# Kernel tuning notes

Hardware: AMD Instinct MI355X
Metric: run time of the kernel (lower is better)

The kernel has to match this reference:

```python
import jax, jax.numpy as jnp
import numpy as np
import math

NEG = -10000.0  # module uses -10000, not -inf


def setup_inputs() -> dict:
    key = jax.random.key(0)
    k1, k2, k3 = jax.random.split(key, 3)
    B, Sq, Sk, H, Hkv, D = 2, 2048, 2048, 16, 4, 64
    q = jax.random.normal(k1, (B, Sq, H, D), dtype=jnp.float32)
    kv = jax.random.normal(k2, (B, Sk, 2, Hkv, D), dtype=jnp.float32)
    key_padding_mask = jax.random.randint(k3, (B, Sk), 0, 2) > 0  # True = valid key
    return {"q": q, "kv": kv, "key_padding_mask": key_padding_mask}


def reference(q, kv, key_padding_mask):
    B, Sq, H, D = q.shape
    Sk, Hkv = kv.shape[1], kv.shape[3]
    if Hkv != H:
        # einops repeat '... hkv d -> ... (hkv g) d': each kv head repeated g times contiguously
        kv = jnp.repeat(kv, H // Hkv, axis=3)
    k, v = kv[:, :, 0], kv[:, :, 1]  # [B, Sk, H, D] each
    scale = 1.0 / math.sqrt(D)
    scores = jnp.einsum('bthd,bshd->bhts', q, k * scale)  # [B, H, Sq, Sk]
    # key padding: additive 0 where valid, -10000 where padded
    pad = jnp.where(key_padding_mask, 0.0, NEG).astype(scores.dtype)
    scores = scores + pad[:, None, None, :]
    # causal mask: cols > rows + Sk - Sq gets replaced (not added) with -10000
    rows = jnp.arange(Sq)[:, None]
    cols = jnp.arange(Sk)[None, :]
    causal_mask = cols > rows + (Sk - Sq)
    scores = jnp.where(causal_mask, NEG, scores)
    attention = jax.nn.softmax(scores, axis=-1).astype(v.dtype)
    # dropout p=0.0 -> identity
    output = jnp.einsum('bhts,bshd->bthd', attention, v)  # [B, Sq, H, D]
    return output
```

## Files before the change

kernel.cpp:

```cpp
#include <hip/hip_runtime.h>
#include <math.h>


typedef __bf16 bf16x4 __attribute__((ext_vector_type(4)));
typedef __bf16 bf16x8 __attribute__((ext_vector_type(8)));
typedef float floatx4 __attribute__((ext_vector_type(4)));
typedef float floatx16 __attribute__((ext_vector_type(16)));

#define B_ 2
#define SQ 2048
#define SK 2048
#define H_ 16
#define HKV 4
#define D_ 64
#define QT 128
#define KT 64
#define PAD 72
#define KVROW 512
#define NEGV (-10000.0f)
#define QSCL 0.18033688f
#define EBIAS 17.3123405f

__global__ __launch_bounds__(256, 2)
void attn_kernel(const float* __restrict__ q,
                 const float* __restrict__ kv,
                 const int* __restrict__ mask,
                 float* __restrict__ out)
{
    __shared__ alignas(16) __bf16 Kt[KT][PAD];
    __shared__ alignas(16) __bf16 Vt[D_][PAD];
    __shared__ alignas(16) __bf16 Pl[4][32][PAD];
    __shared__ float linv[4][32];
    __shared__ float fpart[4][64];
    __shared__ float fw[4][64];
    __shared__ int s_first;

    const int tid  = threadIdx.x;
    const int wave = tid >> 6;
    const int lane = tid & 63;

    if (blockIdx.x >= 512) {
        const int bh = (int)blockIdx.x - 512;
        const int b = bh >> 4, h = bh & 15, hkv = h >> 2;
        if (tid == 0) s_first = SK;
        __syncthreads();
        int local = SK;
        for (int s = tid; s < SK; s += 256)
            if (mask[b * SK + s]) local = min(local, s);
        atomicMin(&s_first, local);
        __syncthreads();
        const int nfirst = s_first;
        if (nfirst == 0) return;

        const float* kvb = kv + (size_t)b * SK * KVROW + hkv * D_;
        const float* vvb = kvb + HKV * D_;
        {
            float a0=0,a1=0,a2=0,a3=0,a4=0,a5=0,a6=0,a7=0;
            const int s0 = wave * 512;
            for (int s = s0; s < s0 + 512; s += 8) {
                a0 += vvb[(size_t)(s+0)*KVROW + lane];
                a1 += vvb[(size_t)(s+1)*KVROW + lane];
                a2 += vvb[(size_t)(s+2)*KVROW + lane];
                a3 += vvb[(size_t)(s+3)*KVROW + lane];
                a4 += vvb[(size_t)(s+4)*KVROW + lane];
                a5 += vvb[(size_t)(s+5)*KVROW + lane];
                a6 += vvb[(size_t)(s+6)*KVROW + lane];
                a7 += vvb[(size_t)(s+7)*KVROW + lane];
            }
            fpart[wave][lane] = ((a0+a1)+(a2+a3)) + ((a4+a5)+(a6+a7));
        }
        __syncthreads();
        const float vtotal = fpart[0][lane]+fpart[1][lane]+fpart[2][lane]+fpart[3][lane];

        for (int R = wave; R < nfirst; R += 4) {
            const float* qrow = q + (((size_t)b * SQ + R) * H_ + h) * D_;
            float mymax = -3.4e38f;
            for (int s = lane; s <= R; s += 64) {
                const float* kp = kvb + (size_t)s * KVROW;
                float dt = 0.f;
                for (int d = 0; d < D_; ++d) dt += qrow[d] * kp[d];
                mymax = fmaxf(mymax, dt * 0.125f + NEGV);
            }
#pragma unroll
            for (int off = 32; off >= 1; off >>= 1)
                mymax = fmaxf(mymax, __shfl_xor(mymax, off, 64));
            const float M = (R < SK - 1) ? fmaxf(mymax, NEGV) : mymax;
            float lsum = 0.f, oacc = 0.f, pref = 0.f;
            for (int s0 = 0; s0 <= R; s0 += 64) {
                int s = s0 + lane;
                float w = 0.f;
                if (s <= R) {
                    const float* kp = kvb + (size_t)s * KVROW;
                    float dt = 0.f;
                    for (int d = 0; d < D_; ++d) dt += qrow[d] * kp[d];
                    w = __expf(dt * 0.125f + NEGV - M);
                    lsum += w;
                }
                fw[wave][lane] = w;
                const int nk = (R - s0 + 1 < 64) ? (R - s0 + 1) : 64;
                for (int j = 0; j < nk; ++j) {
                    const float vj = vvb[(size_t)(s0 + j) * KVROW + lane];
                    oacc += fw[wave][j] * vj;
                    pref += vj;
                }
            }
#pragma unroll
            for (int off = 32; off >= 1; off >>= 1)
                lsum += __shfl_xor(lsum, off, 64);
            const float wn   = __expf(NEGV - M);
            const float ltot = lsum + wn * (float)(SK - 1 - R);
            out[(((size_t)b * SQ + R) * H_ + h) * D_ + lane] =
                (oacc + wn * (vtotal - pref)) / ltot;
        }
        return;
    }

    const int half = lane >> 5;
    const int nn   = lane & 31;

    const int id = (int)blockIdx.x;
    const int bh = id & 31;
    const int y  = id >> 5;
    const int qt = (y < 8) ? 15 - y : y - 8;
    const int b = bh >> 4, h = bh & 15, hkv = h >> 2;
    const int q0 = qt * QT;
    const int qrow_g = q0 + wave * 32 + nn;

    bf16x8 bq[4];
    {
        const float* qp = q + (((size_t)b * SQ + qrow_g) * H_ + h) * D_;
#pragma unroll
        for (int ks = 0; ks < 4; ++ks)
#pragma unroll
            for (int j = 0; j < 8; ++j)
                bq[ks][j] = (__bf16)(qp[ks * 16 + half * 8 + j] * QSCL);
    }

    floatx16 o0, o1;
#pragma unroll
    for (int i = 0; i < 16; ++i) { o0[i] = 0.f; o1[i] = 0.f; }
    float lsum = 0.f;

    const int kkey = tid >> 4;
    const int kd   = (tid & 15) * 4;
    const int vkey = (tid & 15) * 4;
    const int vd   = (tid >> 4) * 4;

    const float* kvb = kv + (size_t)b * SK * KVROW + hkv * D_;

    float4 kreg[4], vreg[4];
    int mreg = 0;

    auto prefetch = [&](int kt) {
        const float* kb = kvb + (size_t)kt * KT * KVROW;
#pragma unroll
        for (int i = 0; i < 4; ++i)
            kreg[i] = *(const float4*)(kb + (kkey + 16 * i) * KVROW + kd);
        const float* vb = kb + HKV * D_;
#pragma unroll
        for (int i = 0; i < 4; ++i)
            vreg[i] = *(const float4*)(vb + (vkey + i) * KVROW + vd);
        mreg = mask[b * SK + kt * KT + lane];
    };

    auto stage = [&]() {
#pragma unroll
        for (int i = 0; i < 4; ++i) {
            bf16x4 t = { (__bf16)kreg[i].x, (__bf16)kreg[i].y,
                         (__bf16)kreg[i].z, (__bf16)kreg[i].w };
            *(bf16x4*)&Kt[kkey + 16 * i][kd] = t;
        }
        const float* vf = (const float*)vreg;
#pragma unroll
        for (int j = 0; j < 4; ++j) {
            bf16x4 t = { (__bf16)vf[0*4+j], (__bf16)vf[1*4+j],
                         (__bf16)vf[2*4+j], (__bf16)vf[3*4+j] };
            *(bf16x4*)&Vt[vd + j][vkey] = t;
        }
    };

    const int nkt = 2 * (qt + 1);
    prefetch(0);

    for (int kt = 0; kt < nkt; ++kt) {
        stage();
        const unsigned long long kept = __ballot(mreg != 0);
        __syncthreads();
        if (kt + 1 < nkt) prefetch(kt + 1);

        const int k0 = kt * KT;
        const bool skipw = (kt == 2*qt + 1) && (wave < 2);
        const bool dg    = (kt == 2*qt) ? (wave < 2) : (kt == 2*qt + 1);

        if (!skipw) {
#pragma unroll
            for (int t2 = 0; t2 < 2; ++t2) {
                floatx16 cst;
#pragma unroll
                for (int i = 0; i < 16; ++i) cst[i] = 0.f;
#pragma unroll
                for (int ks = 0; ks < 4; ++ks) {
                    bf16x8 ak = *(const bf16x8*)&Kt[t2*32 + nn][ks*16 + half*8];
                    cst = __builtin_amdgcn_mfma_f32_32x32x16_bf16(ak, bq[ks], cst, 0, 0, 0);
                }
#pragma unroll
                for (int rq = 0; rq < 4; ++rq) {
                    const int mb = t2*32 + rq*8 + half*4;
                    const unsigned bits = (unsigned)(kept >> mb);
                    bf16x4 pk;
#pragma unroll
                    for (int r = 0; r < 4; ++r) {
                        float p = __builtin_amdgcn_exp2f(cst[rq*4 + r] - EBIAS);
                        if (!((bits >> r) & 1u)) p = 0.f;
                        if (dg && (k0 + mb + r > qrow_g)) p = 0.f;
                        lsum += p;
                        pk[r] = (__bf16)p;
                    }
                    *(bf16x4*)&Pl[wave][nn][mb] = pk;
                }
            }
            bf16x8 ap[4];
#pragma unroll
            for (int ks = 0; ks < 4; ++ks)
                ap[ks] = *(const bf16x8*)&Pl[wave][nn][ks*16 + half*8];
#pragma unroll
            for (int ks = 0; ks < 4; ++ks) {
                bf16x8 bv0 = *(const bf16x8*)&Vt[nn][ks*16 + half*8];
                o0 = __builtin_amdgcn_mfma_f32_32x32x16_bf16(ap[ks], bv0, o0, 0, 0, 0);
                bf16x8 bv1 = *(const bf16x8*)&Vt[32 + nn][ks*16 + half*8];
                o1 = __builtin_amdgcn_mfma_f32_32x32x16_bf16(ap[ks], bv1, o1, 0, 0, 0);
            }
        }
        __syncthreads();
    }

    lsum += __shfl_xor(lsum, 32, 64);
    linv[wave][nn] = (lsum > 0.f) ? 1.f / lsum : 0.f;
#pragma unroll
    for (int rq = 0; rq < 4; ++rq) {
        const int m0 = rq * 8 + half * 4;
        floatx4 li = *(const floatx4*)&linv[wave][m0];
#pragma unroll
        for (int r = 0; r < 4; ++r) {
            if (li[r] != 0.f) {
                const int row = q0 + wave * 32 + m0 + r;
                float* op = out + (((size_t)b * SQ + row) * H_ + h) * D_ + nn;
                op[0]  = o0[rq*4 + r] * li[r];
                op[32] = o1[rq*4 + r] * li[r];
            }
        }
    }
}

extern "C" void kernel_launch(void* const* d_in, const int* in_sizes, int n_in,
                              void* d_out, int out_size, void* d_ws, size_t ws_size,
                              hipStream_t stream) {
    const float* q   = (const float*)d_in[0];
    const float* kv  = (const float*)d_in[1];
    const int* mask  = (const int*)d_in[2];
    float* out       = (float*)d_out;
    attn_kernel<<<dim3(512 + B_ * H_), 256, 0, stream>>>(q, kv, mask, out);
}
```

Measured before the change: 128.9 us.

## Halve query tile and split key tile across wave pairs with LDS reduction

The query tile shrinks from 128 to 64 rows, doubling the block count to 1024 plus 32 fallback blocks. The four waves now form a 2x2 grid: two query halves times two key halves of each 64-key tile. Partial outputs and row sums are combined through a shared-memory reduction unioned with the K/V staging buffers. Launch bounds move to 4 blocks per CU and the special blocks run first. The aim is better occupancy and load balance, at the cost of each K/V tile being loaded twice as often per query row and an extra end-of-kernel reduction.

New measurement: 136.7 us. 1.06x slower.

```diff
diff --git a/kernel.cpp b/kernel.cpp
--- a/kernel.cpp
+++ b/kernel.cpp
@@ -13,34 +13,39 @@
 #define H_ 16
 #define HKV 4
 #define D_ 64
-#define QT 128
+#define QT 64
 #define KT 64
-#define PAD 72
+#define PADK 72
+#define PADP 40
 #define KVROW 512
 #define NEGV (-10000.0f)
 #define QSCL 0.18033688f
 #define EBIAS 17.3123405f
 
-__global__ __launch_bounds__(256, 2)
+__global__ __launch_bounds__(256, 4)
 void attn_kernel(const float* __restrict__ q,
                  const float* __restrict__ kv,
                  const int* __restrict__ mask,
                  float* __restrict__ out)
 {
-    __shared__ alignas(16) __bf16 Kt[KT][PAD];
-    __shared__ alignas(16) __bf16 Vt[D_][PAD];
-    __shared__ alignas(16) __bf16 Pl[4][32][PAD];
-    __shared__ float linv[4][32];
-    __shared__ float fpart[4][64];
-    __shared__ float fw[4][64];
+    __shared__ union {
+        struct { __bf16 Kt[KT][PADK]; __bf16 Vt[D_][PADK]; } m;
+        float Ored[2][32][64];
+        struct { float part[4][64]; float w[4][64]; } f;
+    } u;
+    __shared__ alignas(16) __bf16 Pl[4][32][PADP];
+    __shared__ float lpart[2][2][32];
+    __shared__ float linv[2][32];
     __shared__ int s_first;
 
     const int tid  = threadIdx.x;
     const int wave = tid >> 6;
     const int lane = tid & 63;
-
-    if (blockIdx.x >= 512) {
-        const int bh = (int)blockIdx.x - 512;
+    const int half = lane >> 5;
+    const int nn   = lane & 31;
+
+    if (blockIdx.x < 32) {
+        const int bh = (int)blockIdx.x;
         const int b = bh >> 4, h = bh & 15, hkv = h >> 2;
         if (tid == 0) s_first = SK;
         __syncthreads();
@@ -67,10 +72,11 @@
                 a6 += vvb[(size_t)(s+6)*KVROW + lane];
                 a7 += vvb[(size_t)(s+7)*KVROW + lane];
             }
-            fpart[wave][lane] = ((a0+a1)+(a2+a3)) + ((a4+a5)+(a6+a7));
-        }
-        __syncthreads();
-        const float vtotal = fpart[0][lane]+fpart[1][lane]+fpart[2][lane]+fpart[3][lane];
+            u.f.part[wave][lane] = ((a0+a1)+(a2+a3)) + ((a4+a5)+(a6+a7));
+        }
+        __syncthreads();
+        const float vtotal = u.f.part[0][lane] + u.f.part[1][lane]
+                           + u.f.part[2][lane] + u.f.part[3][lane];
 
         for (int R = wave; R < nfirst; R += 4) {
             const float* qrow = q + (((size_t)b * SQ + R) * H_ + h) * D_;
@@ -96,11 +102,11 @@
                     w = __expf(dt * 0.125f + NEGV - M);
                     lsum += w;
                 }
-                fw[wave][lane] = w;
+                u.f.w[wave][lane] = w;
                 const int nk = (R - s0 + 1 < 64) ? (R - s0 + 1) : 64;
                 for (int j = 0; j < nk; ++j) {
                     const float vj = vvb[(size_t)(s0 + j) * KVROW + lane];
-                    oacc += fw[wave][j] * vj;
+                    oacc += u.f.w[wave][j] * vj;
                     pref += vj;
                 }
             }
@@ -115,16 +121,17 @@
         return;
     }
 
-    const int half = lane >> 5;
-    const int nn   = lane & 31;
-
-    const int id = (int)blockIdx.x;
+    const int id = (int)blockIdx.x - 32;
     const int bh = id & 31;
     const int y  = id >> 5;
-    const int qt = (y < 8) ? 15 - y : y - 8;
+    const int kg = y >> 3, jj = y & 7;
+    const int qt = (kg == 0) ? 31 - jj : (kg == 1) ? jj : (kg == 2) ? 23 - jj : 8 + jj;
     const int b = bh >> 4, h = bh & 15, hkv = h >> 2;
     const int q0 = qt * QT;
-    const int qrow_g = q0 + wave * 32 + nn;
+
+    const int qh = wave & 1;
+    const int kh = wave >> 1;
+    const int qrow_g = q0 + qh * 32 + nn;
 
     bf16x8 bq[4];
     {
@@ -168,18 +175,18 @@
         for (int i = 0; i < 4; ++i) {
             bf16x4 t = { (__bf16)kreg[i].x, (__bf16)kreg[i].y,
                          (__bf16)kreg[i].z, (__bf16)kreg[i].w };
-            *(bf16x4*)&Kt[kkey + 16 * i][kd] = t;
+            *(bf16x4*)&u.m.Kt[kkey + 16 * i][kd] = t;
         }
         const float* vf = (const float*)vreg;
 #pragma unroll
         for (int j = 0; j < 4; ++j) {
             bf16x4 t = { (__bf16)vf[0*4+j], (__bf16)vf[1*4+j],
                          (__bf16)vf[2*4+j], (__bf16)vf[3*4+j] };
-            *(bf16x4*)&Vt[vd + j][vkey] = t;
+            *(bf16x4*)&u.m.Vt[vd + j][vkey] = t;
         }
     };
 
-    const int nkt = 2 * (qt + 1);
+    const int nkt = qt + 1;
     prefetch(0);
 
     for (int kt = 0; kt < nkt; ++kt) {
@@ -189,64 +196,75 @@
         if (kt + 1 < nkt) prefetch(kt + 1);
 
         const int k0 = kt * KT;
-        const bool skipw = (kt == 2*qt + 1) && (wave < 2);
-        const bool dg    = (kt == 2*qt) ? (wave < 2) : (kt == 2*qt + 1);
-
-        if (!skipw) {
-#pragma unroll
-            for (int t2 = 0; t2 < 2; ++t2) {
-                floatx16 cst;
-#pragma unroll
-                for (int i = 0; i < 16; ++i) cst[i] = 0.f;
-#pragma unroll
-                for (int ks = 0; ks < 4; ++ks) {
-                    bf16x8 ak = *(const bf16x8*)&Kt[t2*32 + nn][ks*16 + half*8];
-                    cst = __builtin_amdgcn_mfma_f32_32x32x16_bf16(ak, bq[ks], cst, 0, 0, 0);
-                }
-#pragma unroll
-                for (int rq = 0; rq < 4; ++rq) {
-                    const int mb = t2*32 + rq*8 + half*4;
-                    const unsigned bits = (unsigned)(kept >> mb);
-                    bf16x4 pk;
-#pragma unroll
-                    for (int r = 0; r < 4; ++r) {
-                        float p = __builtin_amdgcn_exp2f(cst[rq*4 + r] - EBIAS);
-                        if (!((bits >> r) & 1u)) p = 0.f;
-                        if (dg && (k0 + mb + r > qrow_g)) p = 0.f;
-                        lsum += p;
-                        pk[r] = (__bf16)p;
-                    }
-                    *(bf16x4*)&Pl[wave][nn][mb] = pk;
-                }
-            }
-            bf16x8 ap[4];
-#pragma unroll
-            for (int ks = 0; ks < 4; ++ks)
-                ap[ks] = *(const bf16x8*)&Pl[wave][nn][ks*16 + half*8];
+        const bool dg = (kt == qt);
+        if (!(dg && wave == 2)) {
+            floatx16 cst;
+#pragma unroll
+            for (int i = 0; i < 16; ++i) cst[i] = 0.f;
 #pragma unroll
             for (int ks = 0; ks < 4; ++ks) {
-                bf16x8 bv0 = *(const bf16x8*)&Vt[nn][ks*16 + half*8];
-                o0 = __builtin_amdgcn_mfma_f32_32x32x16_bf16(ap[ks], bv0, o0, 0, 0, 0);
-                bf16x8 bv1 = *(const bf16x8*)&Vt[32 + nn][ks*16 + half*8];
-                o1 = __builtin_amdgcn_mfma_f32_32x32x16_bf16(ap[ks], bv1, o1, 0, 0, 0);
+                bf16x8 ak = *(const bf16x8*)&u.m.Kt[kh*32 + nn][ks*16 + half*8];
+                cst = __builtin_amdgcn_mfma_f32_32x32x16_bf16(ak, bq[ks], cst, 0, 0, 0);
+            }
+#pragma unroll
+            for (int g = 0; g < 4; ++g) {
+                const int mloc = 8*g + 4*half;
+                const unsigned bits = (unsigned)(kept >> (kh*32 + mloc));
+                bf16x4 pk;
+#pragma unroll
+                for (int r = 0; r < 4; ++r) {
+                    float p = __builtin_amdgcn_exp2f(cst[g*4 + r] - EBIAS);
+                    if (!((bits >> r) & 1u)) p = 0.f;
+                    if (dg && (k0 + kh*32 + mloc + r > qrow_g)) p = 0.f;
+                    lsum += p;
+                    pk[r] = (__bf16)p;
+                }
+                *(bf16x4*)&Pl[wave][nn][mloc] = pk;
+            }
+            bf16x8 ap[2];
+#pragma unroll
+            for (int ks2 = 0; ks2 < 2; ++ks2)
+                ap[ks2] = *(const bf16x8*)&Pl[wave][nn][ks2*16 + half*8];
+#pragma unroll
+            for (int ks2 = 0; ks2 < 2; ++ks2) {
+                bf16x8 bv0 = *(const bf16x8*)&u.m.Vt[nn][kh*32 + ks2*16 + half*8];
+                o0 = __builtin_amdgcn_mfma_f32_32x32x16_bf16(ap[ks2], bv0, o0, 0, 0, 0);
+                bf16x8 bv1 = *(const bf16x8*)&u.m.Vt[32 + nn][kh*32 + ks2*16 + half*8];
+                o1 = __builtin_amdgcn_mfma_f32_32x32x16_bf16(ap[ks2], bv1, o1, 0, 0, 0);
             }
         }
         __syncthreads();
     }
 
     lsum += __shfl_xor(lsum, 32, 64);
-    linv[wave][nn] = (lsum > 0.f) ? 1.f / lsum : 0.f;
-#pragma unroll
-    for (int rq = 0; rq < 4; ++rq) {
-        const int m0 = rq * 8 + half * 4;
-        floatx4 li = *(const floatx4*)&linv[wave][m0];
-#pragma unroll
-        for (int r = 0; r < 4; ++r) {
-            if (li[r] != 0.f) {
-                const int row = q0 + wave * 32 + m0 + r;
-                float* op = out + (((size_t)b * SQ + row) * H_ + h) * D_ + nn;
-                op[0]  = o0[rq*4 + r] * li[r];
-                op[32] = o1[rq*4 + r] * li[r];
+    lpart[kh][qh][nn] = lsum;
+    __syncthreads();
+    if (kh == 0) {
+        const float l = lpart[0][qh][nn] + lpart[1][qh][nn];
+        linv[qh][nn] = (l > 0.f) ? 1.f / l : 0.f;
+#pragma unroll
+        for (int g = 0; g < 4; ++g)
+#pragma unroll
+            for (int r = 0; r < 4; ++r) {
+                const int m = 4*half + 8*g + r;
+                u.Ored[qh][m][nn]      = o0[g*4 + r];
+                u.Ored[qh][m][32 + nn] = o1[g*4 + r];
+            }
+    }
+    __syncthreads();
+    if (kh == 1) {
+#pragma unroll
+        for (int g = 0; g < 4; ++g) {
+            floatx4 li = *(const floatx4*)&linv[qh][8*g + 4*half];
+#pragma unroll
+            for (int r = 0; r < 4; ++r) {
+                if (li[r] != 0.f) {
+                    const int m = 4*half + 8*g + r;
+                    const int row = q0 + qh*32 + m;
+                    float* op = out + (((size_t)b * SQ + row) * H_ + h) * D_ + nn;
+                    op[0]  = (u.Ored[qh][m][nn]      + o0[g*4 + r]) * li[r];
+                    op[32] = (u.Ored[qh][m][32 + nn] + o1[g*4 + r]) * li[r];
+                }
             }
         }
     }
@@ -259,5 +277,5 @@
     const float* kv  = (const float*)d_in[1];
     const int* mask  = (const int*)d_in[2];
     float* out       = (float*)d_out;
-    attn_kernel<<<dim3(512 + B_ * H_), 256, 0, stream>>>(q, kv, mask, out);
+    attn_kernel<<<dim3(32 + 1024), 256, 0, stream>>>(q, kv, mask, out);
 }
```
